# Kernel tuning notes

Hardware: AMD Instinct MI355X
Metric: run time of the kernel (lower is better)

The kernel has to match this reference:

```python
import jax, jax.numpy as jnp
import numpy as np
import math

H = 512        # hidden_dim
DEPTH = 5
KS = 3         # kernel size
DELTA = 0.1
M = 104        # timestamp == seq_len
NC = 5
B = 512
BN_EPS = 1e-5


def setup_inputs() -> dict:
    key = jax.random.key(0)
    ks = jax.random.split(key, 16)
    inp = {}
    inp['x'] = jax.random.normal(ks[0], (B, 1, M), dtype=jnp.float32)
    # CausalCNN: depth conv layers (first is 1->H, rest H->H), each followed by BN
    inp['conv_w0'] = jax.random.normal(ks[1], (H, 1, KS), dtype=jnp.float32) * (1.0 / np.sqrt(KS))
    inp['conv_b0'] = jnp.zeros((H,), jnp.float32)
    inp['conv_w'] = jax.random.normal(ks[2], (DEPTH - 1, H, H, KS), dtype=jnp.float32) * (1.0 / np.sqrt(H * KS))
    inp['conv_b'] = jnp.zeros((DEPTH - 1, H), jnp.float32)
    inp['bn_gamma'] = jnp.ones((DEPTH, H), jnp.float32)
    inp['bn_beta'] = jnp.zeros((DEPTH, H), jnp.float32)
    # input_proj
    inp['proj_w'] = jax.random.normal(ks[3], (H, H), dtype=jnp.float32) * (1.0 / np.sqrt(H))
    inp['proj_b'] = jnp.zeros((H,), jnp.float32)
    # ZOH layers: A = -0.01*I + 0.001*randn, B = 0.01*randn [H,1], C = 0.01*randn [1,H]
    eye = jnp.eye(H, dtype=jnp.float32)
    inp['A_all'] = -0.01 * eye[None] + 0.001 * jax.random.normal(ks[4], (DEPTH, H, H), dtype=jnp.float32)
    inp['B_all'] = 0.01 * jax.random.normal(ks[5], (DEPTH, H, 1), dtype=jnp.float32)
    inp['C_all'] = 0.01 * jax.random.normal(ks[6], (DEPTH, 1, H), dtype=jnp.float32)
    # fc_temp: Linear(H,H) -> BN1d(H) -> GELU -> Dropout(eval) -> Linear(H,NC)
    inp['fc1_w'] = jax.random.normal(ks[7], (H, H), dtype=jnp.float32) * (1.0 / np.sqrt(H))
    inp['fc1_b'] = jnp.zeros((H,), jnp.float32)
    inp['fc_bn_gamma'] = jnp.ones((H,), jnp.float32)
    inp['fc_bn_beta'] = jnp.zeros((H,), jnp.float32)
    inp['fc2_w'] = jax.random.normal(ks[8], (NC, H), dtype=jnp.float32) * (1.0 / np.sqrt(H))
    inp['fc2_b'] = jnp.zeros((NC,), jnp.float32)
    return inp


def _causal_conv(x, w, b):
    # x: [B, Cin, T], w: [Cout, Cin, K] -> left-pad K-1 (equivalent to pad both + trim right)
    y = jax.lax.conv_general_dilated(x, w, window_strides=(1,), padding=[(KS - 1, 0)],
                                     dimension_numbers=('NCH', 'OIH', 'NCH'))
    return y + b[None, :, None]


def _bn_ct(x, g, b):
    # BatchNorm1d over [B, C, T], batch statistics (training-mode normalization)
    m = x.mean(axis=(0, 2), keepdims=True)
    v = x.var(axis=(0, 2), keepdims=True)
    return g[None, :, None] * (x - m) * jax.lax.rsqrt(v + BN_EPS) + b[None, :, None]


def _pos_encoding(T, d):
    pos = jnp.arange(T, dtype=jnp.float32)[:, None]
    div = jnp.exp(jnp.arange(0, d, 2, dtype=jnp.float32) * (-math.log(10000.0) / d))
    pe = jnp.zeros((T, d), jnp.float32)
    pe = pe.at[:, 0::2].set(jnp.sin(pos * div))
    pe = pe.at[:, 1::2].set(jnp.cos(pos * div))
    return pe


def _zoh_kbar(A, Bv, Cv):
    # A: [H,H], Bv: [H,1], Cv: [1,H] -> normalized K_bar [M]
    A_bar = jax.scipy.linalg.expm(DELTA * A)
    I = jnp.eye(H, dtype=A.dtype)
    A_inv = jnp.linalg.inv(A + 0.001 * I)
    B_bar = A_inv @ (A_bar - I) @ (DELTA * Bv)  # [H,1]
    # term_k = C @ A_bar^k @ B_bar; sequential vector recurrence replaces matrix powers
    def step(v, _):
        term = (Cv @ v)[0, 0]
        return A_bar @ v, term
    _, terms = jax.lax.scan(step, B_bar, None, length=M)  # [M]
    Kb = jnp.flip(terms, axis=0)
    return Kb / (jnp.linalg.norm(Kb) + 1e-6)


def reference(x, conv_w0, conv_b0, conv_w, conv_b, bn_gamma, bn_beta, proj_w, proj_b,
              A_all, B_all, C_all, fc1_w, fc1_b, fc_bn_gamma, fc_bn_beta, fc2_w, fc2_b):
    # CausalCNN
    h = jax.nn.relu(_bn_ct(_causal_conv(x, conv_w0, conv_b0), bn_gamma[0], bn_beta[0]))
    for i in range(DEPTH - 1):
        h = jax.nn.relu(_bn_ct(_causal_conv(h, conv_w[i], conv_b[i]), bn_gamma[i + 1], bn_beta[i + 1]))
    h = jnp.transpose(h, (0, 2, 1))  # [B, T, H]
    # positional encoding + input projection
    h = h + _pos_encoding(M, H)[None]
    h = jnp.einsum('bth,oh->bto', h, proj_w) + proj_b
    # stacked ZOH kernels: each layer multiplies x by its normalized K_bar along time
    Ks = jax.vmap(_zoh_kbar)(A_all, B_all, C_all)  # [DEPTH, M]
    h = h * jnp.prod(Ks, axis=0)[None, :, None]
    # mean pool over time, then fc_temp (BN with batch stats, dropout = identity/eval)
    h = h.mean(axis=1)  # [B, H]
    h = jnp.dot(h, fc1_w.T) + fc1_b
    m = h.mean(axis=0, keepdims=True)
    v = h.var(axis=0, keepdims=True)
    h = fc_bn_gamma * (h - m) * jax.lax.rsqrt(v + BN_EPS) + fc_bn_beta
    h = jax.nn.gelu(h, approximate=False)
    logits = jnp.dot(h, fc2_w.T) + fc2_b  # [B, NC]
    return logits
```

## Files before the change

kernel.cpp:

```cpp
#include <hip/hip_runtime.h>
#include <cstdio>
#include <cmath>
#include <cstdint>

constexpr int BM = 512 * 104;
constexpr float BN_EPS = 1e-5f;

constexpr size_t SZ_BF   = (size_t)BM * 512 * 2;
constexpr size_t SZ_MAT5 = (size_t)5 * 512 * 512 * 4;
constexpr size_t OFF_YB0 = 0;
constexpr size_t OFF_YB1 = OFF_YB0 + SZ_BF;
constexpr size_t OFF_WT2 = OFF_YB1 + SZ_BF;
constexpr size_t OFF_X   = OFF_WT2 + 6291456;
constexpr size_t OFF_T1  = OFF_X   + SZ_MAT5;
constexpr size_t OFF_T2  = OFF_T1  + SZ_MAT5;
constexpr size_t OFF_E   = OFF_T2  + SZ_MAT5;
constexpr size_t OFF_MW  = OFF_E   + SZ_MAT5;
constexpr size_t OFF_P2  = OFF_MW  + SZ_MAT5;
constexpr size_t OFF_P4  = OFF_P2  + SZ_MAT5;
constexpr size_t OFF_ROWT= OFF_P4  + SZ_MAT5;
constexpr size_t OFF_COLS= OFF_ROWT + 655360;
constexpr size_t OFF_COLS2=OFF_COLS + 655360;
constexpr size_t OFF_PIVI= OFF_COLS2 + 655360;
constexpr size_t OFF_PJT = OFF_PIVI + 81920;
constexpr size_t OFF_F1T = OFF_PJT + 1048576;
constexpr size_t OFF_G   = OFF_F1T + 1048576;
constexpr size_t OFF_POOL= OFF_G   + 1048576;
constexpr size_t OFF_Z   = OFF_POOL + 1048576;
constexpr size_t OFF_ST  = OFF_Z   + 1048576;
constexpr size_t OFF_U   = OFF_ST  + 49152;
constexpr size_t OFF_SV  = OFF_U   + 10240;
constexpr size_t OFF_V   = OFF_SV  + 10240;
constexpr size_t OFF_WV  = OFF_V   + 81920;
constexpr size_t OFF_S   = OFF_WV  + 133120;
constexpr size_t WS_NEED = OFF_S + 512;

__device__ __forceinline__ float bf2f(unsigned short u) {
    union { uint32_t i; float f; } x; x.i = (uint32_t)u << 16; return x.f;
}
__device__ __forceinline__ unsigned short f2bf(float f) {
    union { float f; uint32_t i; } x; x.f = f;
    uint32_t r = x.i + 0x7FFFu + ((x.i >> 16) & 1u);
    return (unsigned short)(r >> 16);
}

typedef __bf16 bf16x8 __attribute__((ext_vector_type(8)));
typedef float  f32x4  __attribute__((ext_vector_type(4)));

__device__ __forceinline__ void gld16(const void* g, void* l) {
    __builtin_amdgcn_global_load_lds((const __attribute__((address_space(1))) uint32_t*)g,
                                     (__attribute__((address_space(3))) uint32_t*)l, 16, 0, 0);
}

__global__ void k_build(const float* __restrict__ Aall, float* __restrict__ X, float* __restrict__ MW,
                        float* __restrict__ COLSa, const float* __restrict__ Call, float* __restrict__ WV)
{
    long i = (long)blockIdx.x * 256 + threadIdx.x;
    float a = Aall[i];
    X[i] = 0.1f * a;
    int z = (int)(i >> 18);
    int rc = (int)(i & 262143);
    int r = rc >> 9, c = rc & 511;
    float mw = a + ((r == c) ? 0.001f : 0.0f);
    MW[i] = mw;
    if (c < 64) COLSa[(long)z * 32768 + r * 64 + c] = mw;
    if (i < 2560) WV[(i >> 9) * 6656 + (i & 511)] = Call[i];
}

__global__ __launch_bounds__(256) void k_mm(
    const float* __restrict__ A, long sA, int lda,
    const float* __restrict__ Bm, long sB, int ldb,
    float* __restrict__ C, long sC, int ldc,
    int K, int mode,
    const float* __restrict__ aux, long sAux,
    const float* __restrict__ aux2, float* __restrict__ Cp,
    double* __restrict__ st1, double* __restrict__ st2, int pc)
{
    __shared__ float sm[2 * 32 * 68];
    float* As = sm;
    float* Bs = sm + 32 * 68;
    int z = blockIdx.z;
    A  += (long)z * sA;
    Bm += (long)z * sB;
    C  += (long)z * sC;
    if (aux) aux += (long)z * sAux;
    int m0 = blockIdx.x * 64, n0 = blockIdx.y * 64;
    int tid = threadIdx.x;
    int tx = tid & 15, ty = tid >> 4;
    float acc[4][4] = {};
    for (int k0 = 0; k0 < K; k0 += 32) {
        __syncthreads();
#pragma unroll
        for (int it = 0; it < 2; ++it) {
            int s = it * 256 + tid;
            int mm = s >> 3, k4 = (s & 7) * 4;
            float4 v = *(const float4*)&A[(long)(m0 + mm) * lda + k0 + k4];
            As[(k4 + 0) * 68 + mm] = v.x;
            As[(k4 + 1) * 68 + mm] = v.y;
            As[(k4 + 2) * 68 + mm] = v.z;
            As[(k4 + 3) * 68 + mm] = v.w;
        }
#pragma unroll
        for (int it = 0; it < 2; ++it) {
            int s = it * 256 + tid;
            int kk = s >> 4, n4 = (s & 15) * 4;
            *(float4*)&Bs[kk * 68 + n4] = *(const float4*)&Bm[(long)(k0 + kk) * ldb + n0 + n4];
        }
        __syncthreads();
#pragma unroll 8
        for (int kk = 0; kk < 32; ++kk) {
            float4 a = *(const float4*)&As[kk * 68 + ty * 4];
            float4 b = *(const float4*)&Bs[kk * 68 + tx * 4];
            float av[4] = {a.x, a.y, a.z, a.w};
            float bv[4] = {b.x, b.y, b.z, b.w};
#pragma unroll
            for (int i = 0; i < 4; ++i)
#pragma unroll
                for (int j = 0; j < 4; ++j)
                    acc[i][j] = fmaf(av[i], bv[j], acc[i][j]);
        }
    }
    float sc2 = (mode == 5) ? aux2[0] : 0.0f;
    float cs1[4] = {0, 0, 0, 0}, cs2[4] = {0, 0, 0, 0};
#pragma unroll
    for (int i = 0; i < 4; ++i) {
        int row = m0 + ty * 4 + i;
        int col0 = n0 + tx * 4;
        long base = (long)row * ldc + col0;
        float v[4];
#pragma unroll
        for (int j = 0; j < 4; ++j) v[j] = acc[i][j];
        if (mode == 1) {
            for (int j = 0; j < 4; ++j) {
                int col = col0 + j;
                v[j] = v[j] + 2.0f * aux[(long)row * 512 + col] + ((row == col) ? 1.0f : 0.0f);
            }
        } else if (mode == 2) {
            for (int j = 0; j < 4; ++j)
                v[j] = v[j] + aux[(long)row * 512 + col0 + j];
        } else if (mode == 3) {
            bool inP = (col0 >= pc && col0 < pc + 64);
            if (inP)
                for (int j = 0; j < 4; ++j) v[j] = aux[row * 64 + (col0 + j - pc)];
        } else if (mode == 5) {
            for (int j = 0; j < 4; ++j) v[j] += aux[col0 + j] * sc2;
        } else if (mode == 7) {
            float pv[4];
            for (int j = 0; j < 4; ++j) {
                int col = col0 + j;
                pv[j] = ((row == col) ? 0.5f : 0.0f) + aux[(long)row * 512 + col] * (1.0f / 6.0f)
                        + v[j] * (1.0f / 24.0f);
            }
            *(float4*)&Cp[base] = make_float4(pv[0], pv[1], pv[2], pv[3]);
        } else if (mode == 8) {
            for (int j = 0; j < 4; ++j) {
                v[j] += aux[col0 + j];
                cs1[j] += v[j]; cs2[j] += v[j] * v[j];
            }
        }
        *(float4*)&C[base] = make_float4(v[0], v[1], v[2], v[3]);
    }
    if (mode == 8) {
        __syncthreads();
        float* s1s = sm;
        float* s2s = sm + 1024;
#pragma unroll
        for (int j = 0; j < 4; ++j) {
            s1s[ty * 64 + tx * 4 + j] = cs1[j];
            s2s[ty * 64 + tx * 4 + j] = cs2[j];
        }
        __syncthreads();
        if (tid < 64) {
            double a = 0.0, b = 0.0;
#pragma unroll
            for (int t = 0; t < 16; ++t) { a += s1s[t * 64 + tid]; b += s2s[t * 64 + tid]; }
            atomicAdd(&st1[n0 + tid], a);
            atomicAdd(&st2[n0 + tid], b);
        }
    }
}

__global__ __launch_bounds__(256) void k_elim(
    const float* __restrict__ COLSc, const float* __restrict__ ROWT,
    float* __restrict__ MW, float* __restrict__ COLSn, int pr, int pcn)
{
    int z = blockIdx.z;
    COLSc += (long)z * 32768; ROWT += (long)z * 32768;
    MW += (long)z * 262144; COLSn += (long)z * 32768;
    int m0 = blockIdx.x * 64, n0 = blockIdx.y * 64;
    int tid = threadIdx.x;
    if (m0 == pr) {
        for (int it = 0; it < 16; ++it) {
            int idx = it * 256 + tid;
            int r = idx >> 6, c = idx & 63;
            float v = ROWT[r * 512 + n0 + c];
            MW[(long)(pr + r) * 512 + n0 + c] = v;
            if (n0 == pcn) COLSn[(pr + r) * 64 + c] = v;
        }
        return;
    }
    __shared__ float As[64 * 68];
    __shared__ float Bs[64 * 68];
    {
        int m = tid >> 2, kb = (tid & 3) * 16;
#pragma unroll
        for (int u = 0; u < 4; ++u) {
// ... 99 lines not shown
                for (int u = 0; u < 16; ++u) {
                    int c = c0 + u;
                    float val = mat[i * 65 + c] - f * mat[j * 65 + c];
                    if (c == j) val = -f * dd;
                    mat[i * 65 + c] = val;
                }
            }
        }
        __syncthreads();
    }
    if (tid == 0) {
        for (int c = 0; c < 64; ++c) arr[c] = c;
        for (int j = 63; j >= 0; --j) { int r = perm[j]; int t = arr[j]; arr[j] = arr[r]; arr[r] = t; }
    }
    __syncthreads();
    float* Pg = PIVI + z * 4096;
    for (int it = 0; it < 16; ++it) {
        int idx = it * 256 + tid;
        int r = idx >> 6, c = idx & 63;
        Pg[r * 64 + c] = mat[r * 65 + arr[c]];
    }
}

__global__ void k_matvecA(const float* __restrict__ A, long sA,
                          const float* __restrict__ x, long sx,
                          float* __restrict__ y, long sy,
                          const float* __restrict__ sub, long ssub,
                          float alpha, float beta, int accum)
{
    int row = blockIdx.x, z = blockIdx.y, lane = threadIdx.x;
    A += (long)z * sA; x += (long)z * sx; y += (long)z * sy;
    if (sub) sub += (long)z * ssub;
    const float* ar = A + (long)row * 512;
    double acc = 0.0;
#pragma unroll
    for (int m = 0; m < 8; ++m) {
        int k = lane + m * 64;
        acc += (double)ar[k] * (double)x[k];
    }
    for (int off = 32; off; off >>= 1) acc += __shfl_down(acc, off);
    if (lane == 0) {
        float val = alpha * (float)acc + beta * x[row];
        if (sub) val = sub[row] - val;
        if (accum) y[row] += val; else y[row] = val;
    }
}

struct VWT { long a[8]; long x[8]; long y[8]; float al[8]; float be[8]; int ty[8]; };
__global__ void k_vw(const char* __restrict__ ws, VWT T)
{
    int g = blockIdx.x, z = blockIdx.y, t = blockIdx.z;
    int lane = threadIdx.x;
    const float* A = (const float*)(ws + T.a[t]) + (long)z * 262144;
    int ty = T.ty[t];
    long vs = ty ? 6656 : 4096;
    const float* x = (const float*)(ws + T.x[t]) + (long)z * vs;
    float* yv = (float*)(ws + T.y[t]) + (long)z * vs;
    if (ty == 0) {
        float xm[8];
#pragma unroll
        for (int m = 0; m < 8; ++m) xm[m] = x[lane + m * 64];
        float alpha = T.al[t], beta = T.be[t];
        for (int r0 = 0; r0 < 64; ++r0) {
            int row = g * 64 + r0;
            const float* ar = A + (long)row * 512;
            double acc = 0.0;
#pragma unroll
            for (int m = 0; m < 8; ++m) acc += (double)ar[lane + m * 64] * (double)xm[m];
            for (int off = 32; off; off >>= 1) acc += __shfl_down(acc, off);
            if (lane == 0) yv[row] = alpha * (float)acc + beta * x[row];
        }
    } else {
        __shared__ float xl[512];
#pragma unroll
        for (int m = 0; m < 8; ++m) xl[lane + m * 64] = x[lane + m * 64];
        __syncthreads();
        int c = g * 64 + lane;
        double acc = 0.0;
#pragma unroll 8
        for (int j = 0; j < 512; ++j) acc += (double)A[(long)j * 512 + c] * (double)xl[j];
        yv[c] = (float)acc;
    }
}

__global__ __launch_bounds__(512) void k_termsk(const float* __restrict__ WV, const float* __restrict__ V,
                                                float* __restrict__ svec)
{
    __shared__ float tl[520];
    __shared__ float invn[5];
    __shared__ float red[2];
    int tid = threadIdx.x;
    for (int t = tid; t < 520; t += 512) {
        int z = t / 104, d = t - z * 104;
        int j = d >> 3, i = d & 7;
        const float* wp = WV + z * 6656 + j * 512;
        const float* vp = V + z * 4096 + i * 512;
        float acc = 0.0f;
#pragma unroll 8
        for (int k = 0; k < 512; ++k) acc += wp[k] * vp[k];
        tl[t] = acc;
    }
    __syncthreads();
    int w = tid >> 6, lane = tid & 63;
    if (w < 5) {
        float a = tl[w * 104 + lane]; a = a * a;
        if (lane < 40) { float b = tl[w * 104 + 64 + lane]; a += b * b; }
#pragma unroll
        for (int off = 32; off; off >>= 1) a += __shfl_down(a, off);
        if (lane == 0) invn[w] = 1.0f / (sqrtf(a) + 1e-6f);
    }
    __syncthreads();
    float s = 0.0f;
    if (tid < 104) {
        s = 1.0f;
        for (int l = 0; l < 5; ++l) s *= tl[l * 104 + (103 - tid)] * invn[l];
        svec[tid] = s;
    }
    if (tid < 128) {
        float v = (tid < 104) ? s : 0.0f;
#pragma unroll
        for (int off = 32; off; off >>= 1) v += __shfl_down(v, off);
        if ((tid & 63) == 0) red[tid >> 6] = v;
    }
    __syncthreads();
    if (tid == 0) svec[104] = (red[0] + red[1]) * (1.0f / 104.0f);
}

__global__ void k_conv0(const float* __restrict__ x, const float* __restrict__ w0, const float* __restrict__ b0,
                        unsigned short* __restrict__ y, double* __restrict__ s1g, double* __restrict__ s2g)
{
    int b = blockIdx.x;
    int c = blockIdx.y * 256 + threadIdx.x;
    float w_0 = w0[c * 3 + 0], w_1 = w0[c * 3 + 1], w_2 = w0[c * 3 + 2], bb = b0[c];
    const float* xb = x + b * 104;
    unsigned short* yb = y + (long)b * 104 * 512 + c;
    float xm2 = 0.0f, xm1 = 0.0f;
    float s1 = 0.0f, s2 = 0.0f;
    for (int t = 0; t < 104; ++t) {
        float x0 = xb[t];
        float v = w_0 * xm2 + w_1 * xm1 + w_2 * x0 + bb;
        yb[t * 512] = f2bf(v);
        s1 += v; s2 += v * v;
        xm2 = xm1; xm1 = x0;
    }
    atomicAdd(&s1g[c], (double)s1);
    atomicAdd(&s2g[c], (double)s2);
}

__global__ void k_wt2(const float* __restrict__ W, unsigned short* __restrict__ Wt2)
{
    int co = blockIdx.x, l = blockIdx.y, tid = threadIdx.x;
    const float* src = W + (long)(l * 512 + co) * 512 * 3;
    unsigned short* dst = Wt2 + (long)l * 3 * 262144 + ((long)co << 9);
#pragma unroll
    for (int q = 0; q < 2; ++q) {
        int ci = tid * 2 + q;
        float f0 = src[ci * 3 + 0], f1 = src[ci * 3 + 1], f2 = src[ci * 3 + 2];
        dst[ci] = f2bf(f0);
        dst[262144 + ci] = f2bf(f1);
        dst[524288 + ci] = f2bf(f2);
    }
}

__global__ __launch_bounds__(256) void k_convm(
    const unsigned short* __restrict__ act,
    const unsigned short* __restrict__ Wt2,
    const float* __restrict__ bias,
    const double* __restrict__ STin,
    const float* __restrict__ gam, const float* __restrict__ bet,
    unsigned short* __restrict__ yout,
    double* __restrict__ s1g, double* __restrict__ s2g)
{
    __shared__ __align__(16) unsigned short As[130 * 32];
    __shared__ __align__(16) unsigned short Bs[3 * 128 * 32];
    __shared__ float SCs[512];
    __shared__ float SHs[512];
    int tid = threadIdx.x;
    int m0 = blockIdx.x * 128, co0 = blockIdx.y * 128;
    int w = tid >> 6, lane = tid & 63;
    int wr = (w >> 1) * 64, wc = (w & 1) * 64;
    int fr = lane & 15, fkb = (lane >> 4) * 8, quad = lane >> 4;

    const double invN = 1.0 / (double)BM;
    for (int c = tid; c < 512; c += 256) {
        double mn = STin[c] * invN;
        double var = STin[512 + c] * invN - mn * mn;
        double rs = 1.0 / sqrt(var + (double)BN_EPS);
        double scd = (double)gam[c] * rs;
        SCs[c] = (float)scd;
        SHs[c] = (float)((double)bet[c] - mn * scd);
    }

    bool valid[4][3];
#pragma unroll
    for (int i = 0; i < 4; ++i) {
        int R = m0 + wr + i * 16 + fr;
        int t = R % 104;
#pragma unroll
        for (int tau = 0; tau < 3; ++tau) valid[i][tau] = (t + tau >= 2);
    }
    int ka = (tid & 3) * 8;
    int g0 = m0 - 2 + (tid >> 2); if (g0 < 0) g0 = 0;
    int g1 = m0 + 62 + (tid >> 2);
    int g2 = m0 + 126 + (tid >> 2);
    const unsigned short* pa0 = act + (long)g0 * 512 + ka;
    const unsigned short* pa1 = act + (long)g1 * 512 + ka;
    const unsigned short* pa2 = act + (long)g2 * 512 + ka;
    const unsigned short* pb[6];
#pragma unroll
    for (int it = 0; it < 6; ++it) {
        int c = it * 256 + tid;
        int tau = c >> 9, r = (c >> 2) & 127, kq = (c & 3) * 8;
        pb[it] = Wt2 + ((long)tau << 18) + ((long)(co0 + r) << 9) + kq;
    }

    f32x4 zero4 = {0.f, 0.f, 0.f, 0.f};
    f32x4 acc[4][4];
#pragma unroll
    for (int i = 0; i < 4; ++i)
#pragma unroll
        for (int j = 0; j < 4; ++j) acc[i][j] = zero4;
    bf16x8 zer = {0, 0, 0, 0, 0, 0, 0, 0};

#pragma unroll 1
    for (int s = 0; s < 16; ++s) {
        int ci0 = s * 32;
        int cb = ci0 + ka;
        __syncthreads();
#pragma unroll
        for (int it = 0; it < 6; ++it)
            gld16(pb[it] + ci0, &Bs[it * 2048 + tid * 8]);
        float4 s0 = *(const float4*)&SCs[cb], s1v = *(const float4*)&SCs[cb + 4];
        float4 h0 = *(const float4*)&SHs[cb], h1v = *(const float4*)&SHs[cb + 4];
        float ss[8] = {s0.x, s0.y, s0.z, s0.w, s1v.x, s1v.y, s1v.z, s1v.w};
        float hh[8] = {h0.x, h0.y, h0.z, h0.w, h1v.x, h1v.y, h1v.z, h1v.w};
        int nrep = (tid < 8) ? 3 : 2;
        const unsigned short* pas[3] = {pa0, pa1, pa2};
#pragma unroll
        for (int rep = 0; rep < 3; ++rep) {
            if (rep < nrep) {
                uint4 v = *(const uint4*)(pas[rep] + ci0);
                unsigned short u[8];
                u[0] = (unsigned short)(v.x & 0xFFFF); u[1] = (unsigned short)(v.x >> 16);
                u[2] = (unsigned short)(v.y & 0xFFFF); u[3] = (unsigned short)(v.y >> 16);
                u[4] = (unsigned short)(v.z & 0xFFFF); u[5] = (unsigned short)(v.z >> 16);
                u[6] = (unsigned short)(v.w & 0xFFFF); u[7] = (unsigned short)(v.w >> 16);
                unsigned short o[8];
#pragma unroll
                for (int q = 0; q < 8; ++q)
                    o[q] = f2bf(fmaxf(fmaf(bf2f(u[q]), ss[q], hh[q]), 0.0f));
                uint4 pk;
                pk.x = (uint32_t)o[0] | ((uint32_t)o[1] << 16);
                pk.y = (uint32_t)o[2] | ((uint32_t)o[3] << 16);
                pk.z = (uint32_t)o[4] | ((uint32_t)o[5] << 16);
                pk.w = (uint32_t)o[6] | ((uint32_t)o[7] << 16);
                *(uint4*)&As[rep * 2048 + tid * 8] = pk;
            }
        }
        __syncthreads();
#pragma unroll
        for (int tau = 0; tau < 3; ++tau) {
            bf16x8 af[4], bfr[4];
#pragma unroll
            for (int i = 0; i < 4; ++i) {
                bf16x8 raw = *(const bf16x8*)&As[(wr + i * 16 + fr + tau) * 32 + fkb];
                af[i] = valid[i][tau] ? raw : zer;
            }
#pragma unroll
            for (int j = 0; j < 4; ++j)
                bfr[j] = *(const bf16x8*)&Bs[tau * 4096 + (wc + j * 16 + fr) * 32 + fkb];
#pragma unroll
            for (int i = 0; i < 4; ++i)
#pragma unroll
                for (int j = 0; j < 4; ++j)
                    acc[i][j] = __builtin_amdgcn_mfma_f32_16x16x32_bf16(af[i], bfr[j], acc[i][j], 0, 0, 0);
        }
    }
    float bcol[4], s1[4] = {0, 0, 0, 0}, s2[4] = {0, 0, 0, 0};
#pragma unroll
    for (int jt = 0; jt < 4; ++jt) bcol[jt] = bias[co0 + wc + jt * 16 + fr];
#pragma unroll
    for (int i = 0; i < 4; ++i) {
        int rbase = m0 + wr + i * 16 + quad * 4;
#pragma unroll
        for (int jt = 0; jt < 4; ++jt) {
            int col = co0 + wc + jt * 16 + fr;
#pragma unroll
            for (int r = 0; r < 4; ++r) {
                float v = acc[i][jt][r] + bcol[jt];
                yout[(long)(rbase + r) * 512 + col] = f2bf(v);
                s1[jt] += v; s2[jt] += v * v;
            }
        }
    }
#pragma unroll
    for (int jt = 0; jt < 4; ++jt) {
        s1[jt] += __shfl_xor(s1[jt], 16); s1[jt] += __shfl_xor(s1[jt], 32);
        s2[jt] += __shfl_xor(s2[jt], 16); s2[jt] += __shfl_xor(s2[jt], 32);
    }
    __syncthreads();
    float* st = (float*)As;
    if (lane < 16) {
#pragma unroll
        for (int jt = 0; jt < 4; ++jt) {
            st[w * 64 + jt * 16 + lane] = s1[jt];
            st[256 + w * 64 + jt * 16 + lane] = s2[jt];
        }
    }
    __syncthreads();
    if (tid < 128) {
        int half = tid >> 6, cl = tid & 63;
        float a = st[half * 64 + cl] + st[(half + 2) * 64 + cl];
        float b = st[256 + half * 64 + cl] + st[256 + (half + 2) * 64 + cl];
        atomicAdd(&s1g[co0 + tid], (double)a);
        atomicAdd(&s2g[co0 + tid], (double)b);
    }
}

__global__ void k_pool(const unsigned short* __restrict__ y4, const double* __restrict__ ST4,
                       const float* __restrict__ gam, const float* __restrict__ bet,
                       const float* __restrict__ svec, float* __restrict__ g)
{
    __shared__ float sl[104];
    int b = blockIdx.x;
    int c = blockIdx.y * 256 + threadIdx.x;
    if (threadIdx.x < 104) sl[threadIdx.x] = svec[threadIdx.x];
    __syncthreads();
    const double invN = 1.0 / (double)BM;
    double mn = ST4[c] * invN;
    double var = ST4[512 + c] * invN - mn * mn;
    double rs = 1.0 / sqrt(var + (double)BN_EPS);
    double scd = (double)gam[c] * rs;
    float sc = (float)scd, sh = (float)((double)bet[c] - mn * scd);
    int he = c & ~1;
    float div = expf((float)he * (-0.017988946039015984f));
    float acc = 0.0f;
    const unsigned short* yb = y4 + (long)b * 104 * 512 + c;
    for (int t = 0; t < 104; ++t) {
        float v = bf2f(yb[t * 512]);
        float hn = fmaxf(fmaf(v, sc, sh), 0.0f);
        float arg = (float)t * div;
        float pe = (c & 1) ? cosf(arg) : sinf(arg);
        acc += sl[t] * (hn + pe);
    }
    g[(long)b * 512 + c] = acc * (1.0f / 104.0f);
}

__global__ void k_t512(const float* __restrict__ in0, float* __restrict__ out0,
                       const float* __restrict__ in1, float* __restrict__ out1)
{
    __shared__ float tile[64 * 68];
    const float* in = blockIdx.z ? in1 : in0;
    float* outp = blockIdx.z ? out1 : out0;
    int bx = blockIdx.x, by = blockIdx.y;
    int tid = threadIdx.x;
    for (int it = 0; it < 4; ++it) {
        int s = it * 256 + tid;
        int r = s >> 4, c4 = (s & 15) * 4;
        *(float4*)&tile[r * 68 + c4] = *(const float4*)&in[(long)(bx * 64 + r) * 512 + by * 64 + c4];
    }
    __syncthreads();
    for (int it = 0; it < 4; ++it) {
        int s = it * 256 + tid;
        int r = s >> 4, c4 = (s & 15) * 4;
        float4 v;
        v.x = tile[(c4 + 0) * 68 + r];
        v.y = tile[(c4 + 1) * 68 + r];
        v.z = tile[(c4 + 2) * 68 + r];
        v.w = tile[(c4 + 3) * 68 + r];
        *(float4*)&outp[(long)(by * 64 + r) * 512 + bx * 64 + c4] = v;
    }
}

__global__ __launch_bounds__(256) void k_final(const float* __restrict__ zin, const double* __restrict__ st,
                                               const float* __restrict__ gam, const float* __restrict__ bet,
                                               const float* __restrict__ w2, const float* __restrict__ b2,
                                               float* __restrict__ outp)
{
    __shared__ float red[256];
    int b = blockIdx.x, tid = threadIdx.x;
    int oo[2] = { tid, tid + 256 };
    float gv[2];
#pragma unroll
    for (int q = 0; q < 2; ++q) {
        int o = oo[q];
        double m = st[o] * (1.0 / 512.0);
        double var = st[512 + o] * (1.0 / 512.0) - m * m;
        double rs = 1.0 / sqrt(var + (double)BN_EPS);
        float xn = (float)(((double)zin[(long)b * 512 + o] - m) * rs * (double)gam[o] + (double)bet[o]);
        gv[q] = 0.5f * xn * (1.0f + erff(xn * 0.70710678118654752f));
    }
    for (int n = 0; n < 5; ++n) {
        float p = gv[0] * w2[n * 512 + oo[0]] + gv[1] * w2[n * 512 + oo[1]];
        red[tid] = p;
        __syncthreads();
        for (int off = 128; off; off >>= 1) { if (tid < off) red[tid] += red[tid + off]; __syncthreads(); }
        if (tid == 0) outp[b * 5 + n] = red[0] + b2[n];
        __syncthreads();
    }
}

static void mm(hipStream_t s, int Mt, int Nt, int z,
               const float* A, long sA, int lda,
               const float* B, long sB, int ldb,
               float* C, long sC, int ldc,
               int K, int mode,
               const float* aux = nullptr, long sAux = 0, const float* aux2 = nullptr,
               float* Cp = nullptr, double* st1 = nullptr, double* st2 = nullptr, int pc = 0)
{
    dim3 g(Mt, Nt, z);
    k_mm<<<g, 256, 0, s>>>(A, sA, lda, B, sB, ldb, C, sC, ldc, K, mode, aux, sAux, aux2, Cp, st1, st2, pc);
}

extern "C" void kernel_launch(void* const* d_in, const int* in_sizes, int n_in,
                              void* d_out, int out_size, void* d_ws, size_t ws_size,
                              hipStream_t stream)
{
    (void)in_sizes; (void)n_in; (void)out_size;
    const float* x       = (const float*)d_in[0];
    const float* conv_w0 = (const float*)d_in[1];
    const float* conv_b0 = (const float*)d_in[2];
    const float* conv_w  = (const float*)d_in[3];
    const float* conv_b  = (const float*)d_in[4];
    const float* bn_g    = (const float*)d_in[5];
    const float* bn_b    = (const float*)d_in[6];
    const float* proj_w  = (const float*)d_in[7];
    const float* proj_b  = (const float*)d_in[8];
    const float* A_all   = (const float*)d_in[9];
    const float* B_all   = (const float*)d_in[10];
    const float* C_all   = (const float*)d_in[11];
    const float* fc1_w   = (const float*)d_in[12];
    const float* fc1_b   = (const float*)d_in[13];
    const float* fbn_g   = (const float*)d_in[14];
    const float* fbn_b   = (const float*)d_in[15];
    const float* fc2_w   = (const float*)d_in[16];
    const float* fc2_b   = (const float*)d_in[17];
    float* outp = (float*)d_out;
    char* ws = (char*)d_ws;
    if (ws_size < WS_NEED) { printf("ws too small: %zu < %zu\n", ws_size, WS_NEED); return; }

    unsigned short* YB0 = (unsigned short*)(ws + OFF_YB0);
    unsigned short* YB1 = (unsigned short*)(ws + OFF_YB1);
    unsigned short* WT2 = (unsigned short*)(ws + OFF_WT2);
    float* Xb   = (float*)(ws + OFF_X);
    float* T1   = (float*)(ws + OFF_T1);
    float* T2   = (float*)(ws + OFF_T2);
    float* Eb   = (float*)(ws + OFF_E);
    float* MW   = (float*)(ws + OFF_MW);
    float* P2   = (float*)(ws + OFF_P2);
    float* P4   = (float*)(ws + OFF_P4);
    float* ROWT = (float*)(ws + OFF_ROWT);
    float* COLS1= (float*)(ws + OFF_COLS);
    float* COLS2= (float*)(ws + OFF_COLS2);
    float* PIVI = (float*)(ws + OFF_PIVI);
    float* PJT  = (float*)(ws + OFF_PJT);
    float* F1T  = (float*)(ws + OFF_F1T);
    float* G    = (float*)(ws + OFF_G);
    float* POOL = (float*)(ws + OFF_POOL);
    float* Zb   = (float*)(ws + OFF_Z);
    double* ST  = (double*)(ws + OFF_ST);
    float* U    = (float*)(ws + OFF_U);
    float* SV   = (float*)(ws + OFF_SV);
    float* V    = (float*)(ws + OFF_V);
    float* WV   = (float*)(ws + OFF_WV);
    float* SVEC = (float*)(ws + OFF_S);

    const long SM = 262144;
    hipMemsetAsync(ws + OFF_ST, 0, 49152, stream);

    k_wt2<<<dim3(512, 4), 256, 0, stream>>>(conv_w, WT2);
    k_build<<<5120, 256, 0, stream>>>(A_all, Xb, MW, COLS1, C_all, WV);
    for (int p = 0; p < 8; ++p) {
        int pc = p * 64;
        float* Cc = (p & 1) ? COLS2 : COLS1;
        float* Cn = (p & 1) ? COLS1 : COLS2;
        k_inv64<<<5, 256, 0, stream>>>(MW, p, PIVI);
        mm(stream, 1, 8, 5, PIVI, 4096, 64, MW + pc * 512, SM, 512, ROWT, 32768, 512, 64, 3,
           PIVI, 4096, nullptr, nullptr, nullptr, nullptr, pc);
        k_elim<<<dim3(8, 8, 5), 256, 0, stream>>>(Cc, ROWT, MW, Cn, pc, pc + 64);
    }
    mm(stream, 8, 8, 5, Xb, SM, 512, Xb, SM, 512, T2, SM, 512, 512, 7, Xb, SM, nullptr, T1);
    mm(stream, 8, 8, 5, T2, SM, 512, T1, SM, 512, Eb, SM, 512, 512, 2, Xb, SM);
    mm(stream, 8, 8, 5, Eb, SM, 512, Eb, SM, 512, Xb, SM, 512, 512, 1, Eb, SM);
    mm(stream, 8, 8, 5, Xb, SM, 512, Xb, SM, 512, T1, SM, 512, 512, 0);
    mm(stream, 8, 8, 5, T1, SM, 512, T1, SM, 512, T2, SM, 512, 512, 0);
    mm(stream, 8, 8, 5, T2, SM, 512, T2, SM, 512, P2, SM, 512, 512, 0);
    mm(stream, 8, 8, 5, P2, SM, 512, P2, SM, 512, P4, SM, 512, 512, 0);
    k_matvecA<<<dim3(512, 5), 64, 0, stream>>>(Eb, SM, B_all, 512, U, 512, nullptr, 0, 0.1f, 0.0f, 0);
    k_matvecA<<<dim3(512, 5), 64, 0, stream>>>(MW, SM, U, 512, V, 4096, nullptr, 0, 1.0f, 0.0f, 0);
    k_matvecA<<<dim3(512, 5), 64, 0, stream>>>(A_all, SM, V, 4096, SV, 512, U, 512, 1.0f, 0.001f, 0);
    k_matvecA<<<dim3(512, 5), 64, 0, stream>>>(MW, SM, SV, 512, V, 4096, nullptr, 0, 1.0f, 0.0f, 1);
    auto Voff = [](int i) { return (long)(OFF_V + (size_t)i * 2048); };
    auto Woff = [](int j) { return (long)(OFF_WV + (size_t)j * 2048); };
    {
        VWT T = {};
        T.a[0] = OFF_E;  T.x[0] = Voff(0); T.y[0] = Voff(1); T.al[0] = 1; T.be[0] = 1; T.ty[0] = 0;
        T.a[1] = OFF_T2; T.x[1] = Woff(0); T.y[1] = Woff(1); T.ty[1] = 1;
        k_vw<<<dim3(8, 5, 2), 64, 0, stream>>>(ws, T);
    }
    {
        VWT T = {};
        T.a[0] = OFF_X;  T.x[0] = Voff(0); T.y[0] = Voff(2); T.al[0] = 1; T.ty[0] = 0;
        T.a[1] = OFF_X;  T.x[1] = Voff(1); T.y[1] = Voff(3); T.al[1] = 1; T.ty[1] = 0;
        T.a[2] = OFF_P2; T.x[2] = Woff(0); T.y[2] = Woff(2); T.ty[2] = 1;
        T.a[3] = OFF_P2; T.x[3] = Woff(1); T.y[3] = Woff(3); T.ty[3] = 1;
        k_vw<<<dim3(8, 5, 4), 64, 0, stream>>>(ws, T);
    }
    {
        VWT T = {};
        for (int i = 0; i < 4; ++i) {
            T.a[i] = OFF_T1; T.x[i] = Voff(i); T.y[i] = Voff(4 + i); T.al[i] = 1; T.ty[i] = 0;
            T.a[4 + i] = OFF_P4; T.x[4 + i] = Woff(i); T.y[4 + i] = Woff(4 + i); T.ty[4 + i] = 1;
        }
        k_vw<<<dim3(8, 5, 8), 64, 0, stream>>>(ws, T);
    }
    {
        VWT T = {};
        for (int i = 0; i < 4; ++i) {
            T.a[i] = OFF_P4; T.x[i] = Woff(4 + i); T.y[i] = Woff(8 + i); T.ty[i] = 1;
        }
        k_vw<<<dim3(8, 5, 4), 64, 0, stream>>>(ws, T);
    }
    {
        VWT T = {};
        T.a[0] = OFF_P4; T.x[0] = Woff(8); T.y[0] = Woff(12); T.ty[0] = 1;
        k_vw<<<dim3(8, 5, 1), 64, 0, stream>>>(ws, T);
    }
    k_termsk<<<1, 512, 0, stream>>>(WV, V, SVEC);

    k_conv0<<<dim3(512, 2), 256, 0, stream>>>(x, conv_w0, conv_b0, YB0, ST, ST + 512);
    for (int l = 1; l <= 4; ++l) {
        unsigned short* inb  = (l & 1) ? YB0 : YB1;
        unsigned short* outb = (l & 1) ? YB1 : YB0;
        k_convm<<<dim3(416, 4), 256, 0, stream>>>(inb, WT2 + (size_t)(l - 1) * 3 * 262144,
                                                  conv_b + (l - 1) * 512,
                                                  ST + (l - 1) * 1024, bn_g + (l - 1) * 512, bn_b + (l - 1) * 512,
                                                  outb, ST + l * 1024, ST + l * 1024 + 512);
    }
    k_pool<<<dim3(512, 2), 256, 0, stream>>>(YB0, ST + 4 * 1024, bn_g + 4 * 512, bn_b + 4 * 512, SVEC, G);

    k_t512<<<dim3(8, 8, 2), 256, 0, stream>>>(proj_w, PJT, fc1_w, F1T);
    mm(stream, 8, 8, 1, G, 0, 512, PJT, 0, 512, POOL, 0, 512, 512, 5, proj_b, 0, SVEC + 104);
    mm(stream, 8, 8, 1, POOL, 0, 512, F1T, 0, 512, Zb, 0, 512, 512, 8, fc1_b, 0, nullptr, nullptr,
       ST + 5 * 1024, ST + 5 * 1024 + 512);
    k_final<<<512, 256, 0, stream>>>(Zb, ST + 5 * 1024, fbn_g, fbn_b, fc2_w, fc2_b, outp);
}
```

Measured before the change: 1.874 ms.

## Widen conv GEMM tile to 256 output channels with swizzled LDS layout

The causal conv GEMM block tile grows from 128x128 to 128x256 output channels, so each wave computes 4x8 MFMA tiles and the BN+ReLU-transformed activation tile is reused across twice as many output columns. A and B LDS layouts are XOR-swizzled (weights pre-swizzled in k_wt2) to reduce bank conflicts, and the BN+ReLU bf16 conversion uses a packed v_cvt_pk_bf16_f32. Activation global loads are issued before the weight LDS loads. This halves the grid to 832 blocks and raises register and LDS pressure, so occupancy may fall.

```diff
diff --git a/kernel.cpp b/kernel.cpp
--- a/kernel.cpp
+++ b/kernel.cpp
@@ -52,6 +52,17 @@
                                      (__attribute__((address_space(3))) uint32_t*)l, 16, 0, 0);
 }
 
+__device__ __forceinline__ uint32_t bnrelu_pk(uint32_t u, float sc0, float sc1, float sh0, float sh1) {
+    union { uint32_t i; float f; } a, b;
+    a.i = u << 16;
+    b.i = u & 0xFFFF0000u;
+    float x0 = fmaxf(fmaf(a.f, sc0, sh0), 0.0f);
+    float x1 = fmaxf(fmaf(b.f, sc1, sh1), 0.0f);
+    uint32_t r;
+    asm volatile("v_cvt_pk_bf16_f32 %0, %1, %2" : "=v"(r) : "v"(x0), "v"(x1));
+    return r;
+}
+
 __global__ void k_build(const float* __restrict__ Aall, float* __restrict__ X, float* __restrict__ MW,
                         float* __restrict__ COLSa, const float* __restrict__ Call, float* __restrict__ WV)
 {
@@ -457,17 +468,20 @@
     int co = blockIdx.x, l = blockIdx.y, tid = threadIdx.x;
     const float* src = W + (long)(l * 512 + co) * 512 * 3;
     unsigned short* dst = Wt2 + (long)l * 3 * 262144 + ((long)co << 9);
+    int v = (co >> 1) & 3;
 #pragma unroll
     for (int q = 0; q < 2; ++q) {
         int ci = tid * 2 + q;
+        int chunk = (ci >> 3) & 3;
+        int di = (ci & ~31) + (((chunk ^ v) & 3) << 3) + (ci & 7);
         float f0 = src[ci * 3 + 0], f1 = src[ci * 3 + 1], f2 = src[ci * 3 + 2];
-        dst[ci] = f2bf(f0);
-        dst[262144 + ci] = f2bf(f1);
-        dst[524288 + ci] = f2bf(f2);
-    }
-}
-
-__global__ __launch_bounds__(256) void k_convm(
+        dst[di] = f2bf(f0);
+        dst[262144 + di] = f2bf(f1);
+        dst[524288 + di] = f2bf(f2);
+    }
+}
+
+__global__ __launch_bounds__(256, 2) void k_convm(
     const unsigned short* __restrict__ act,
     const unsigned short* __restrict__ Wt2,
     const float* __restrict__ bias,
@@ -477,14 +491,14 @@
     double* __restrict__ s1g, double* __restrict__ s2g)
 {
     __shared__ __align__(16) unsigned short As[130 * 32];
-    __shared__ __align__(16) unsigned short Bs[3 * 128 * 32];
+    __shared__ __align__(16) unsigned short Bs[3 * 256 * 32];
     __shared__ float SCs[512];
     __shared__ float SHs[512];
     int tid = threadIdx.x;
-    int m0 = blockIdx.x * 128, co0 = blockIdx.y * 128;
+    int m0 = blockIdx.x * 128, co0 = blockIdx.y * 256;
     int w = tid >> 6, lane = tid & 63;
-    int wr = (w >> 1) * 64, wc = (w & 1) * 64;
-    int fr = lane & 15, fkb = (lane >> 4) * 8, quad = lane >> 4;
+    int wr = (w >> 1) * 64, wc = (w & 1) * 128;
+    int fr = lane & 15, quad = lane >> 4;
 
     const double invN = 1.0 / (double)BM;
     for (int c = tid; c < 512; c += 256) {
@@ -504,6 +518,22 @@
 #pragma unroll
         for (int tau = 0; tau < 3; ++tau) valid[i][tau] = (t + tau >= 2);
     }
+
+    int aoff[4][3];
+#pragma unroll
+    for (int i = 0; i < 4; ++i)
+#pragma unroll
+        for (int tau = 0; tau < 3; ++tau) {
+            int r = wr + i * 16 + fr + tau;
+            aoff[i][tau] = r * 32 + (((quad ^ (r >> 1)) & 3) << 3);
+        }
+    int boff[8];
+#pragma unroll
+    for (int j = 0; j < 8; ++j) {
+        int rb = wc + j * 16 + fr;
+        boff[j] = rb * 32 + (((quad ^ (rb >> 1)) & 3) << 3);
+    }
+
     int ka = (tid & 3) * 8;
     int g0 = m0 - 2 + (tid >> 2); if (g0 < 0) g0 = 0;
     int g1 = m0 + 62 + (tid >> 2);
@@ -511,84 +541,84 @@
     const unsigned short* pa0 = act + (long)g0 * 512 + ka;
     const unsigned short* pa1 = act + (long)g1 * 512 + ka;
     const unsigned short* pa2 = act + (long)g2 * 512 + ka;
-    const unsigned short* pb[6];
-#pragma unroll
-    for (int it = 0; it < 6; ++it) {
-        int c = it * 256 + tid;
-        int tau = c >> 9, r = (c >> 2) & 127, kq = (c & 3) * 8;
-        pb[it] = Wt2 + ((long)tau << 18) + ((long)(co0 + r) << 9) + kq;
-    }
+    int wbase = (tid >> 2) * 32 + ((((tid & 3) ^ (tid >> 3)) & 3) << 3);
+    const unsigned short* pbB = Wt2 + ((long)(co0 + (tid >> 2)) << 9) + ka;
 
     f32x4 zero4 = {0.f, 0.f, 0.f, 0.f};
-    f32x4 acc[4][4];
+    f32x4 acc[4][8];
 #pragma unroll
     for (int i = 0; i < 4; ++i)
 #pragma unroll
-        for (int j = 0; j < 4; ++j) acc[i][j] = zero4;
+        for (int j = 0; j < 8; ++j) acc[i][j] = zero4;
     bf16x8 zer = {0, 0, 0, 0, 0, 0, 0, 0};
 
 #pragma unroll 1
     for (int s = 0; s < 16; ++s) {
         int ci0 = s * 32;
+        __syncthreads();
+        uint4 va0 = *(const uint4*)(pa0 + ci0);
+        uint4 va1 = *(const uint4*)(pa1 + ci0);
+        uint4 va2;
+        if (tid < 8) va2 = *(const uint4*)(pa2 + ci0);
+#pragma unroll
+        for (int tau = 0; tau < 3; ++tau)
+#pragma unroll
+            for (int it = 0; it < 4; ++it)
+                gld16(pbB + tau * 262144 + it * 32768 + ci0, &Bs[(tau * 4 + it) * 2048 + tid * 8]);
         int cb = ci0 + ka;
-        __syncthreads();
-#pragma unroll
-        for (int it = 0; it < 6; ++it)
-            gld16(pb[it] + ci0, &Bs[it * 2048 + tid * 8]);
         float4 s0 = *(const float4*)&SCs[cb], s1v = *(const float4*)&SCs[cb + 4];
         float4 h0 = *(const float4*)&SHs[cb], h1v = *(const float4*)&SHs[cb + 4];
-        float ss[8] = {s0.x, s0.y, s0.z, s0.w, s1v.x, s1v.y, s1v.z, s1v.w};
-        float hh[8] = {h0.x, h0.y, h0.z, h0.w, h1v.x, h1v.y, h1v.z, h1v.w};
-        int nrep = (tid < 8) ? 3 : 2;
-        const unsigned short* pas[3] = {pa0, pa1, pa2};
-#pragma unroll
-        for (int rep = 0; rep < 3; ++rep) {
-            if (rep < nrep) {
-                uint4 v = *(const uint4*)(pas[rep] + ci0);
-                unsigned short u[8];
-                u[0] = (unsigned short)(v.x & 0xFFFF); u[1] = (unsigned short)(v.x >> 16);
-                u[2] = (unsigned short)(v.y & 0xFFFF); u[3] = (unsigned short)(v.y >> 16);
-                u[4] = (unsigned short)(v.z & 0xFFFF); u[5] = (unsigned short)(v.z >> 16);
-                u[6] = (unsigned short)(v.w & 0xFFFF); u[7] = (unsigned short)(v.w >> 16);
-                unsigned short o[8];
-#pragma unroll
-                for (int q = 0; q < 8; ++q)
-                    o[q] = f2bf(fmaxf(fmaf(bf2f(u[q]), ss[q], hh[q]), 0.0f));
-                uint4 pk;
-                pk.x = (uint32_t)o[0] | ((uint32_t)o[1] << 16);
-                pk.y = (uint32_t)o[2] | ((uint32_t)o[3] << 16);
-                pk.z = (uint32_t)o[4] | ((uint32_t)o[5] << 16);
-                pk.w = (uint32_t)o[6] | ((uint32_t)o[7] << 16);
-                *(uint4*)&As[rep * 2048 + tid * 8] = pk;
+        {
+            uint4 pk;
+            pk.x = bnrelu_pk(va0.x, s0.x, s0.y, h0.x, h0.y);
+            pk.y = bnrelu_pk(va0.y, s0.z, s0.w, h0.z, h0.w);
+            pk.z = bnrelu_pk(va0.z, s1v.x, s1v.y, h1v.x, h1v.y);
+            pk.w = bnrelu_pk(va0.w, s1v.z, s1v.w, h1v.z, h1v.w);
+            *(uint4*)&As[wbase] = pk;
+            pk.x = bnrelu_pk(va1.x, s0.x, s0.y, h0.x, h0.y);
+            pk.y = bnrelu_pk(va1.y, s0.z, s0.w, h0.z, h0.w);
+            pk.z = bnrelu_pk(va1.z, s1v.x, s1v.y, h1v.x, h1v.y);
+            pk.w = bnrelu_pk(va1.w, s1v.z, s1v.w, h1v.z, h1v.w);
+            *(uint4*)&As[wbase + 2048] = pk;
+            if (tid < 8) {
+                pk.x = bnrelu_pk(va2.x, s0.x, s0.y, h0.x, h0.y);
+                pk.y = bnrelu_pk(va2.y, s0.z, s0.w, h0.z, h0.w);
+                pk.z = bnrelu_pk(va2.z, s1v.x, s1v.y, h1v.x, h1v.y);
+                pk.w = bnrelu_pk(va2.w, s1v.z, s1v.w, h1v.z, h1v.w);
+                *(uint4*)&As[wbase + 4096] = pk;
             }
         }
         __syncthreads();
 #pragma unroll
         for (int tau = 0; tau < 3; ++tau) {
-            bf16x8 af[4], bfr[4];
+            bf16x8 af[4];
 #pragma unroll
             for (int i = 0; i < 4; ++i) {
-                bf16x8 raw = *(const bf16x8*)&As[(wr + i * 16 + fr + tau) * 32 + fkb];
+                bf16x8 raw = *(const bf16x8*)&As[aoff[i][tau]];
                 af[i] = valid[i][tau] ? raw : zer;
             }
-#pragma unroll
-            for (int j = 0; j < 4; ++j)
-                bfr[j] = *(const bf16x8*)&Bs[tau * 4096 + (wc + j * 16 + fr) * 32 + fkb];
+            bf16x8 bfr[8];
+#pragma unroll
+            for (int j = 0; j < 8; ++j)
+                bfr[j] = *(const bf16x8*)&Bs[tau * 8192 + boff[j]];
 #pragma unroll
             for (int i = 0; i < 4; ++i)
 #pragma unroll
-                for (int j = 0; j < 4; ++j)
+                for (int j = 0; j < 8; ++j)
                     acc[i][j] = __builtin_amdgcn_mfma_f32_16x16x32_bf16(af[i], bfr[j], acc[i][j], 0, 0, 0);
         }
     }
-    float bcol[4], s1[4] = {0, 0, 0, 0}, s2[4] = {0, 0, 0, 0};
-#pragma unroll
-    for (int jt = 0; jt < 4; ++jt) bcol[jt] = bias[co0 + wc + jt * 16 + fr];
+    float bcol[8], s1[8], s2[8];
+#pragma unroll
+    for (int jt = 0; jt < 8; ++jt) {
+        bcol[jt] = bias[co0 + wc + jt * 16 + fr];
+        s1[jt] = 0.0f; s2[jt] = 0.0f;
+    }
 #pragma unroll
     for (int i = 0; i < 4; ++i) {
         int rbase = m0 + wr + i * 16 + quad * 4;
 #pragma unroll
-        for (int jt = 0; jt < 4; ++jt) {
+        for (int jt = 0; jt < 8; ++jt) {
             int col = co0 + wc + jt * 16 + fr;
 #pragma unroll
             for (int r = 0; r < 4; ++r) {
@@ -599,7 +629,7 @@
         }
     }
 #pragma unroll
-    for (int jt = 0; jt < 4; ++jt) {
+    for (int jt = 0; jt < 8; ++jt) {
         s1[jt] += __shfl_xor(s1[jt], 16); s1[jt] += __shfl_xor(s1[jt], 32);
         s2[jt] += __shfl_xor(s2[jt], 16); s2[jt] += __shfl_xor(s2[jt], 32);
     }
@@ -607,16 +637,16 @@
     float* st = (float*)As;
     if (lane < 16) {
 #pragma unroll
-        for (int jt = 0; jt < 4; ++jt) {
-            st[w * 64 + jt * 16 + lane] = s1[jt];
-            st[256 + w * 64 + jt * 16 + lane] = s2[jt];
-        }
-    }
-    __syncthreads();
-    if (tid < 128) {
-        int half = tid >> 6, cl = tid & 63;
-        float a = st[half * 64 + cl] + st[(half + 2) * 64 + cl];
-        float b = st[256 + half * 64 + cl] + st[256 + (half + 2) * 64 + cl];
+        for (int jt = 0; jt < 8; ++jt) {
+            st[w * 128 + jt * 16 + lane] = s1[jt];
+            st[512 + w * 128 + jt * 16 + lane] = s2[jt];
+        }
+    }
+    __syncthreads();
+    {
+        int half = tid >> 7, cl = tid & 127;
+        float a = st[half * 128 + cl] + st[(half + 2) * 128 + cl];
+        float b = st[512 + half * 128 + cl] + st[512 + (half + 2) * 128 + cl];
         atomicAdd(&s1g[co0 + tid], (double)a);
         atomicAdd(&s2g[co0 + tid], (double)b);
     }
@@ -837,7 +867,7 @@
     for (int l = 1; l <= 4; ++l) {
         unsigned short* inb  = (l & 1) ? YB0 : YB1;
         unsigned short* outb = (l & 1) ? YB1 : YB0;
-        k_convm<<<dim3(416, 4), 256, 0, stream>>>(inb, WT2 + (size_t)(l - 1) * 3 * 262144,
+        k_convm<<<dim3(416, 2), 256, 0, stream>>>(inb, WT2 + (size_t)(l - 1) * 3 * 262144,
                                                   conv_b + (l - 1) * 512,
                                                   ST + (l - 1) * 1024, bn_g + (l - 1) * 512, bn_b + (l - 1) * 512,
                                                   outb, ST + l * 1024, ST + l * 1024 + 512);
```

Measured after the change: 1.809 ms. -3.5%, faster.

## Double-buffer conv GEMM LDS tiles with XOR swizzle and packed bf16 BN-ReLU

Applied to the files above, without the earlier changes.

The causal-conv GEMM kernel now uses two LDS buffers for the activation and weight tiles. The next k-slice's global loads and BN+ReLU transform are issued while MFMAs run on the current slice, so only one barrier per slice remains. LDS layouts for A and B get an XOR swizzle, with the weight pre-transpose kernel writing swizzled order, to reduce bank conflicts on fragment reads. BN-ReLU packing uses v_cvt_pk_bf16_f32, and MFMA sections raise wave priority. The cost is doubled LDS use and higher register pressure under a launch bound of 2 blocks.

```diff
diff --git a/kernel.cpp b/kernel.cpp
--- a/kernel.cpp
+++ b/kernel.cpp
@@ -52,6 +52,17 @@
                                      (__attribute__((address_space(3))) uint32_t*)l, 16, 0, 0);
 }
 
+__device__ __forceinline__ uint32_t bnrelu_pk(uint32_t u, float sc0, float sc1, float sh0, float sh1) {
+    union { uint32_t i; float f; } a, b;
+    a.i = u << 16;
+    b.i = u & 0xFFFF0000u;
+    float x0 = fmaxf(fmaf(a.f, sc0, sh0), 0.0f);
+    float x1 = fmaxf(fmaf(b.f, sc1, sh1), 0.0f);
+    uint32_t r;
+    asm volatile("v_cvt_pk_bf16_f32 %0, %1, %2" : "=v"(r) : "v"(x0), "v"(x1));
+    return r;
+}
+
 __global__ void k_build(const float* __restrict__ Aall, float* __restrict__ X, float* __restrict__ MW,
                         float* __restrict__ COLSa, const float* __restrict__ Call, float* __restrict__ WV)
 {
@@ -457,17 +468,20 @@
     int co = blockIdx.x, l = blockIdx.y, tid = threadIdx.x;
     const float* src = W + (long)(l * 512 + co) * 512 * 3;
     unsigned short* dst = Wt2 + (long)l * 3 * 262144 + ((long)co << 9);
+    int v = (co >> 1) & 3;
 #pragma unroll
     for (int q = 0; q < 2; ++q) {
         int ci = tid * 2 + q;
+        int chunk = (ci >> 3) & 3;
+        int di = (ci & ~31) + (((chunk ^ v) & 3) << 3) + (ci & 7);
         float f0 = src[ci * 3 + 0], f1 = src[ci * 3 + 1], f2 = src[ci * 3 + 2];
-        dst[ci] = f2bf(f0);
-        dst[262144 + ci] = f2bf(f1);
-        dst[524288 + ci] = f2bf(f2);
-    }
-}
-
-__global__ __launch_bounds__(256) void k_convm(
+        dst[di] = f2bf(f0);
+        dst[262144 + di] = f2bf(f1);
+        dst[524288 + di] = f2bf(f2);
+    }
+}
+
+__global__ __launch_bounds__(256, 2) void k_convm(
     const unsigned short* __restrict__ act,
     const unsigned short* __restrict__ Wt2,
     const float* __restrict__ bias,
@@ -476,15 +490,15 @@
     unsigned short* __restrict__ yout,
     double* __restrict__ s1g, double* __restrict__ s2g)
 {
-    __shared__ __align__(16) unsigned short As[130 * 32];
-    __shared__ __align__(16) unsigned short Bs[3 * 128 * 32];
+    __shared__ __align__(16) unsigned short As[2][130 * 32];
+    __shared__ __align__(16) unsigned short Bs[2][3 * 128 * 32];
     __shared__ float SCs[512];
     __shared__ float SHs[512];
     int tid = threadIdx.x;
     int m0 = blockIdx.x * 128, co0 = blockIdx.y * 128;
     int w = tid >> 6, lane = tid & 63;
     int wr = (w >> 1) * 64, wc = (w & 1) * 64;
-    int fr = lane & 15, fkb = (lane >> 4) * 8, quad = lane >> 4;
+    int fr = lane & 15, quad = lane >> 4;
 
     const double invN = 1.0 / (double)BM;
     for (int c = tid; c < 512; c += 256) {
@@ -504,6 +518,22 @@
 #pragma unroll
         for (int tau = 0; tau < 3; ++tau) valid[i][tau] = (t + tau >= 2);
     }
+
+    int aoff[4][3];
+#pragma unroll
+    for (int i = 0; i < 4; ++i)
+#pragma unroll
+        for (int tau = 0; tau < 3; ++tau) {
+            int r = wr + i * 16 + fr + tau;
+            aoff[i][tau] = r * 32 + (((quad ^ (r >> 1)) & 3) << 3);
+        }
+    int boff[4];
+#pragma unroll
+    for (int j = 0; j < 4; ++j) {
+        int rb = wc + j * 16 + fr;
+        boff[j] = rb * 32 + (((quad ^ (rb >> 1)) & 3) << 3);
+    }
+
     int ka = (tid & 3) * 8;
     int g0 = m0 - 2 + (tid >> 2); if (g0 < 0) g0 = 0;
     int g1 = m0 + 62 + (tid >> 2);
@@ -511,13 +541,8 @@
     const unsigned short* pa0 = act + (long)g0 * 512 + ka;
     const unsigned short* pa1 = act + (long)g1 * 512 + ka;
     const unsigned short* pa2 = act + (long)g2 * 512 + ka;
-    const unsigned short* pb[6];
-#pragma unroll
-    for (int it = 0; it < 6; ++it) {
-        int c = it * 256 + tid;
-        int tau = c >> 9, r = (c >> 2) & 127, kq = (c & 3) * 8;
-        pb[it] = Wt2 + ((long)tau << 18) + ((long)(co0 + r) << 9) + kq;
-    }
+    int wbase = (tid >> 2) * 32 + ((((tid & 3) ^ (tid >> 3)) & 3) << 3);
+    const unsigned short* pbB = Wt2 + ((long)(co0 + (tid >> 2)) << 9) + ka;
 
     f32x4 zero4 = {0.f, 0.f, 0.f, 0.f};
     f32x4 acc[4][4];
@@ -527,60 +552,84 @@
         for (int j = 0; j < 4; ++j) acc[i][j] = zero4;
     bf16x8 zer = {0, 0, 0, 0, 0, 0, 0, 0};
 
+    uint4 vA0, vA1, vA2, vB0, vB1, vB2;
+
+#define LOADA(v0_, v1_, v2_, s_) { int ci0 = (s_) * 32;                       \
+        v0_ = *(const uint4*)(pa0 + ci0);                                     \
+        v1_ = *(const uint4*)(pa1 + ci0);                                     \
+        if (tid < 8) v2_ = *(const uint4*)(pa2 + ci0); }
+
+#define GLDB(buf_, s_) { int ci0 = (s_) * 32;                                 \
+        _Pragma("unroll")                                                     \
+        for (int tau = 0; tau < 3; ++tau) {                                   \
+            gld16(pbB + tau * 262144 + ci0,         &Bs[buf_][tau * 4096 + tid * 8]);          \
+            gld16(pbB + tau * 262144 + 32768 + ci0, &Bs[buf_][tau * 4096 + 2048 + tid * 8]); } }
+
+#define BNW(v0_, v1_, v2_, buf_, s_) { int cb = (s_) * 32 + ka;               \
+        float4 s0 = *(const float4*)&SCs[cb], s1v = *(const float4*)&SCs[cb + 4]; \
+        float4 h0 = *(const float4*)&SHs[cb], h1v = *(const float4*)&SHs[cb + 4]; \
+        uint4 pk;                                                             \
+        pk.x = bnrelu_pk(v0_.x, s0.x, s0.y, h0.x, h0.y);                      \
+        pk.y = bnrelu_pk(v0_.y, s0.z, s0.w, h0.z, h0.w);                      \
+        pk.z = bnrelu_pk(v0_.z, s1v.x, s1v.y, h1v.x, h1v.y);                  \
+        pk.w = bnrelu_pk(v0_.w, s1v.z, s1v.w, h1v.z, h1v.w);                  \
+        *(uint4*)&As[buf_][wbase] = pk;                                       \
+        pk.x = bnrelu_pk(v1_.x, s0.x, s0.y, h0.x, h0.y);                      \
+        pk.y = bnrelu_pk(v1_.y, s0.z, s0.w, h0.z, h0.w);                      \
+        pk.z = bnrelu_pk(v1_.z, s1v.x, s1v.y, h1v.x, h1v.y);                  \
+        pk.w = bnrelu_pk(v1_.w, s1v.z, s1v.w, h1v.z, h1v.w);                  \
+        *(uint4*)&As[buf_][wbase + 2048] = pk;                                \
+        if (tid < 8) {                                                        \
+            pk.x = bnrelu_pk(v2_.x, s0.x, s0.y, h0.x, h0.y);                  \
+            pk.y = bnrelu_pk(v2_.y, s0.z, s0.w, h0.z, h0.w);                  \
+            pk.z = bnrelu_pk(v2_.z, s1v.x, s1v.y, h1v.x, h1v.y);              \
+            pk.w = bnrelu_pk(v2_.w, s1v.z, s1v.w, h1v.z, h1v.w);              \
+            *(uint4*)&As[buf_][wbase + 4096] = pk; } }
+
+#define COMPUTE(buf_) {                                                       \
+        _Pragma("unroll")                                                     \
+        for (int tau = 0; tau < 3; ++tau) {                                   \
+            bf16x8 af[4];                                                     \
+            _Pragma("unroll")                                                 \
+            for (int i = 0; i < 4; ++i) {                                     \
+                bf16x8 raw = *(const bf16x8*)&As[buf_][aoff[i][tau]];         \
+                af[i] = valid[i][tau] ? raw : zer; }                          \
+            bf16x8 bfr[4];                                                    \
+            _Pragma("unroll")                                                 \
+            for (int j = 0; j < 4; ++j)                                       \
+                bfr[j] = *(const bf16x8*)&Bs[buf_][tau * 4096 + boff[j]];     \
+            __builtin_amdgcn_s_setprio(1);                                    \
+            _Pragma("unroll")                                                 \
+            for (int i = 0; i < 4; ++i)                                       \
+                _Pragma("unroll")                                             \
+                for (int j = 0; j < 4; ++j)                                   \
+                    acc[i][j] = __builtin_amdgcn_mfma_f32_16x16x32_bf16(af[i], bfr[j], acc[i][j], 0, 0, 0); \
+            __builtin_amdgcn_s_setprio(0); } }
+
+    __syncthreads();
+    LOADA(vA0, vA1, vA2, 0);
+    GLDB(0, 0);
+    BNW(vA0, vA1, vA2, 0, 0);
+    LOADA(vB0, vB1, vB2, 1);
+    __syncthreads();
+
 #pragma unroll 1
-    for (int s = 0; s < 16; ++s) {
-        int ci0 = s * 32;
-        int cb = ci0 + ka;
-        __syncthreads();
-#pragma unroll
-        for (int it = 0; it < 6; ++it)
-            gld16(pb[it] + ci0, &Bs[it * 2048 + tid * 8]);
-        float4 s0 = *(const float4*)&SCs[cb], s1v = *(const float4*)&SCs[cb + 4];
-        float4 h0 = *(const float4*)&SHs[cb], h1v = *(const float4*)&SHs[cb + 4];
-        float ss[8] = {s0.x, s0.y, s0.z, s0.w, s1v.x, s1v.y, s1v.z, s1v.w};
-        float hh[8] = {h0.x, h0.y, h0.z, h0.w, h1v.x, h1v.y, h1v.z, h1v.w};
-        int nrep = (tid < 8) ? 3 : 2;
-        const unsigned short* pas[3] = {pa0, pa1, pa2};
-#pragma unroll
-        for (int rep = 0; rep < 3; ++rep) {
-            if (rep < nrep) {
-                uint4 v = *(const uint4*)(pas[rep] + ci0);
-                unsigned short u[8];
-                u[0] = (unsigned short)(v.x & 0xFFFF); u[1] = (unsigned short)(v.x >> 16);
-                u[2] = (unsigned short)(v.y & 0xFFFF); u[3] = (unsigned short)(v.y >> 16);
-                u[4] = (unsigned short)(v.z & 0xFFFF); u[5] = (unsigned short)(v.z >> 16);
-                u[6] = (unsigned short)(v.w & 0xFFFF); u[7] = (unsigned short)(v.w >> 16);
-                unsigned short o[8];
-#pragma unroll
-                for (int q = 0; q < 8; ++q)
-                    o[q] = f2bf(fmaxf(fmaf(bf2f(u[q]), ss[q], hh[q]), 0.0f));
-                uint4 pk;
-                pk.x = (uint32_t)o[0] | ((uint32_t)o[1] << 16);
-                pk.y = (uint32_t)o[2] | ((uint32_t)o[3] << 16);
-                pk.z = (uint32_t)o[4] | ((uint32_t)o[5] << 16);
-                pk.w = (uint32_t)o[6] | ((uint32_t)o[7] << 16);
-                *(uint4*)&As[rep * 2048 + tid * 8] = pk;
-            }
-        }
-        __syncthreads();
-#pragma unroll
-        for (int tau = 0; tau < 3; ++tau) {
-            bf16x8 af[4], bfr[4];
-#pragma unroll
-            for (int i = 0; i < 4; ++i) {
-                bf16x8 raw = *(const bf16x8*)&As[(wr + i * 16 + fr + tau) * 32 + fkb];
-                af[i] = valid[i][tau] ? raw : zer;
-            }
-#pragma unroll
-            for (int j = 0; j < 4; ++j)
-                bfr[j] = *(const bf16x8*)&Bs[tau * 4096 + (wc + j * 16 + fr) * 32 + fkb];
-#pragma unroll
-            for (int i = 0; i < 4; ++i)
-#pragma unroll
-                for (int j = 0; j < 4; ++j)
-                    acc[i][j] = __builtin_amdgcn_mfma_f32_16x16x32_bf16(af[i], bfr[j], acc[i][j], 0, 0, 0);
-        }
-    }
+    for (int su = 0; su < 8; ++su) {
+        int s = su * 2;
+        if (s < 15) { GLDB(1, s + 1); BNW(vB0, vB1, vB2, 1, s + 1); }
+        if (s < 14) LOADA(vA0, vA1, vA2, s + 2);
+        COMPUTE(0);
+        __syncthreads();
+        if (s < 14) { GLDB(0, s + 2); BNW(vA0, vA1, vA2, 0, s + 2); }
+        if (s < 13) LOADA(vB0, vB1, vB2, s + 3);
+        COMPUTE(1);
+        __syncthreads();
+    }
+#undef LOADA
+#undef GLDB
+#undef BNW
+#undef COMPUTE
+
     float bcol[4], s1[4] = {0, 0, 0, 0}, s2[4] = {0, 0, 0, 0};
 #pragma unroll
     for (int jt = 0; jt < 4; ++jt) bcol[jt] = bias[co0 + wc + jt * 16 + fr];
@@ -614,9 +663,9 @@
     }
     __syncthreads();
     if (tid < 128) {
-        int half = tid >> 6, cl = tid & 63;
-        float a = st[half * 64 + cl] + st[(half + 2) * 64 + cl];
-        float b = st[256 + half * 64 + cl] + st[256 + (half + 2) * 64 + cl];
+        int w0 = tid >> 6, cl = tid & 63;
+        float a = st[w0 * 64 + cl] + st[(w0 + 2) * 64 + cl];
+        float b = st[256 + w0 * 64 + cl] + st[256 + (w0 + 2) * 64 + cl];
         atomicAdd(&s1g[co0 + tid], (double)a);
         atomicAdd(&s2g[co0 + tid], (double)b);
     }
```

New measurement: 1.881 ms. Within noise of the previous version (+0.4%).
